# Performance work log

Hardware: AMD Instinct MI355X
Metric: run time of the kernel (lower is better)

Reference implementation:

```python
import jax, jax.numpy as jnp
import numpy as np

KH = KW = 3
STRIDE = 1
PAD = 1
DIL = 1


def im2col(x, kh, kw, stride, pad, dil):
    """F.unfold equivalent: x (N,C,H,W) -> (N,C,kh,kw,oh,ow)."""
    n, c, h, w = x.shape
    oh = (h + 2 * pad - dil * (kh - 1) - 1) // stride + 1
    ow = (w + 2 * pad - dil * (kw - 1) - 1) // stride + 1
    xp = jnp.pad(x, ((0, 0), (0, 0), (pad, pad), (pad, pad)))
    rows = []
    for i in range(kh):
        cols = []
        for j in range(kw):
            patch = jax.lax.slice(
                xp,
                (0, 0, i * dil, j * dil),
                (n, c, i * dil + (oh - 1) * stride + 1, j * dil + (ow - 1) * stride + 1),
                (1, 1, stride, stride),
            )  # (N,C,oh,ow)
            cols.append(patch)
        rows.append(jnp.stack(cols, axis=2))  # (N,C,kw,oh,ow)
    return jnp.stack(rows, axis=2)  # (N,C,kh,kw,oh,ow)


def setup_inputs() -> dict:
    key = jax.random.key(0)
    k1, k2, k3, k4 = jax.random.split(key, 4)
    N, Cin, Cout, H, W = 4, 64, 64, 128, 128
    x = jax.random.normal(k1, (N, Cin, H, W), dtype=jnp.float32)
    # adapting kernel: positive values (softmax-like output in EdgeKernel2d)
    kernel = jax.random.uniform(k2, (N, 1, KH, KW, H, W), dtype=jnp.float32, minval=0.01, maxval=1.0)
    fan_in = Cin * KH * KW
    weight = jax.random.normal(k3, (Cout, Cin, KH, KW), dtype=jnp.float32) * (1.0 / np.sqrt(fan_in))
    bias = jax.random.normal(k4, (Cout,), dtype=jnp.float32) * 0.01
    return {"x": x, "kernel": kernel, "weight": weight, "bias": bias}


def reference(x, kernel, weight, bias):
    # im_cols: (N,Cin,kh,kw,oh,ow)
    im_cols = im2col(x, KH, KW, STRIDE, PAD, DIL)
    in_mul_k = im_cols * kernel  # kernel broadcasts over Cin
    # dominate = sum_{k,l} in_mul_k / sum_{k,l} kernel  -> (N,Cin,oh,ow)
    dominate = in_mul_k.sum(axis=(2, 3)) / kernel.sum(axis=(2, 3))
    corrected = in_mul_k + dominate[:, :, None, None] * (1.0 - kernel)
    out = jnp.einsum('ncklhw,ockl->nohw', corrected, weight)
    out = out + bias[None, :, None, None]
    return out
```

## Files before the change

kernel.cpp:

```cpp
#include <hip/hip_runtime.h>
#include <cstddef>
#include <cstdint>

typedef __attribute__((ext_vector_type(8))) short bf16x8;
typedef __attribute__((ext_vector_type(4))) short short4v;
typedef __attribute__((ext_vector_type(4))) float f32x4;

#define NB 4
#define CIN 64
#define COUT 64
#define HH 128
#define WW 128
#define TAPS 9
#define PX 64
#define CCH 16
#define KCH 160
#define KTOT 640
#define STR 164

__device__ __forceinline__ unsigned short f2bf(float f) {
    union { float f; unsigned u; } v; v.f = f;
    unsigned u = v.u + 0x7FFFu + ((v.u >> 16) & 1u);
    return (unsigned short)(u >> 16);
}

__global__ void prep_weight(const float* __restrict__ w, unsigned short* __restrict__ wB) {
    int idx = blockIdx.x * blockDim.x + threadIdx.x;
    if (idx >= COUT * KTOT) return;
    int o = idx / KTOT;
    int kk = idx - o * KTOT;
    int chunk = kk / KCH;
    int kl = kk - chunk * KCH;
    unsigned short v = 0;
    if (kl < CCH * TAPS) {
        int tap = kl >> 4;
        int cl = kl & 15;
        int c = chunk * CCH + cl;
        v = f2bf(w[(o * CIN + c) * TAPS + tap]);
    }
    wB[idx] = v;
}

__launch_bounds__(256)
__global__ void pac_conv(const float* __restrict__ x, const float* __restrict__ Kp,
                         const unsigned short* __restrict__ wB,
                         const float* __restrict__ bias, float* __restrict__ out) {
    __shared__ __align__(16) unsigned short sCorT[PX][STR];
    __shared__ float sK[TAPS][PX];
    __shared__ float sInv[PX];

    const int blk = blockIdx.x;
    const int w0 = (blk & 1) * PX;
    const int h = (blk >> 1) & (HH - 1);
    const int n = blk >> 8;

    const int t = threadIdx.x;
    const int lane = t & 63;
    const int wv = t >> 6;
    const int spx = lane;

    for (int i = t; i < TAPS * PX; i += 256) {
        int tap = i >> 6, px = i & 63;
        sK[tap][px] = Kp[((n * TAPS + tap) * HH + h) * WW + w0 + px];
    }
    for (int i = t; i < PX * 16; i += 256) {
        sCorT[i >> 4][144 + (i & 15)] = 0;
    }
    __syncthreads();
    if (t < PX) {
        float s = 0.f;
        #pragma unroll
        for (int tap = 0; tap < TAPS; ++tap) s += sK[tap][t];
        sInv[t] = 1.0f / s;
    }
    __syncthreads();

    float kreg[TAPS];
    #pragma unroll
    for (int tap = 0; tap < TAPS; ++tap) kreg[tap] = sK[tap][spx];
    const float inv = sInv[spx];

    f32x4 acc[4];
    #pragma unroll
    for (int i = 0; i < 4; ++i) acc[i] = (f32x4){0.f, 0.f, 0.f, 0.f};

    const int o0 = wv * 16;
    const int l15 = lane & 15;
    const int kg = (lane >> 4) * 8;

    for (int chunk = 0; chunk < 4; ++chunk) {
        __syncthreads();
        const int cbase = chunk * CCH;
        #pragma unroll
        for (int it = 0; it < 4; ++it) {
            const int cl = wv + it * 4;
            const float* xb = x + (size_t)(n * CIN + cbase + cl) * (HH * WW);
            float xv[TAPS];
            float s1 = 0.f;
            #pragma unroll
            for (int k = 0; k < 3; ++k) {
                const int hh = h + k - 1;
                const bool hok = (unsigned)hh < (unsigned)HH;
                #pragma unroll
                for (int l = 0; l < 3; ++l) {
                    const int wc = w0 + spx + l - 1;
                    const bool ok = hok && ((unsigned)wc < (unsigned)WW);
                    float v = ok ? xb[hh * WW + wc] : 0.f;
                    xv[k * 3 + l] = v;
                    s1 = fmaf(v, kreg[k * 3 + l], s1);
                }
            }
            const float dom = s1 * inv;
            #pragma unroll
            for (int tap = 0; tap < TAPS; ++tap) {
                sCorT[spx][tap * 16 + cl] = f2bf(fmaf(kreg[tap], xv[tap] - dom, dom));
            }
        }
        __syncthreads();

        const unsigned short* wrow = wB + (size_t)(o0 + l15) * KTOT + chunk * KCH + kg;
        #pragma unroll
        for (int step = 0; step < 5; ++step) {
            const int k0 = step * 32;
            bf16x8 bfrag = *reinterpret_cast<const bf16x8*>(wrow + k0);
            #pragma unroll
            for (int pt = 0; pt < 4; ++pt) {
                const unsigned short* ap = &sCorT[pt * 16 + l15][k0 + kg];
                short4v alo = *reinterpret_cast<const short4v*>(ap);
                short4v ahi = *reinterpret_cast<const short4v*>(ap + 4);
                bf16x8 afrag;
                #pragma unroll
                for (int j = 0; j < 4; ++j) { afrag[j] = alo[j]; afrag[4 + j] = ahi[j]; }
                acc[pt] = __builtin_amdgcn_mfma_f32_16x16x32_bf16(afrag, bfrag, acc[pt], 0, 0, 0);
            }
        }
    }

    __syncthreads();
    float* sOut = reinterpret_cast<float*>(&sCorT[0][0]);
    #pragma unroll
    for (int pt = 0; pt < 4; ++pt) {
        #pragma unroll
        for (int r = 0; r < 4; ++r) {
            const int px = pt * 16 + (lane >> 4) * 4 + r;
            sOut[(o0 + l15) * 65 + px] = acc[pt][r];
        }
    }
    __syncthreads();
    #pragma unroll
    for (int j = 0; j < 16; ++j) {
        const int o = wv * 16 + j;
        out[(((size_t)n * COUT + o) * HH + h) * WW + w0 + spx] = sOut[o * 65 + spx] + bias[o];
    }
}

extern "C" void kernel_launch(void* const* d_in, const int* in_sizes, int n_in,
                              void* d_out, int out_size, void* d_ws, size_t ws_size,
                              hipStream_t stream) {
    const float* x    = (const float*)d_in[0];
    const float* Kp   = (const float*)d_in[1];
    const float* wgt  = (const float*)d_in[2];
    const float* bias = (const float*)d_in[3];
    float* out = (float*)d_out;
    unsigned short* wB = (unsigned short*)d_ws;

    prep_weight<<<(COUT * KTOT + 255) / 256, 256, 0, stream>>>(wgt, wB);

    pac_conv<<<NB * HH * (WW / PX), 256, 0, stream>>>(x, Kp, wB, bias, out);
}
```

Baseline: 33.78 us.

## Batch input loads per wave, pack bf16 pairs, and store MFMA results directly

Each wave now loads four channels at once with branch-free offset loads. Out-of-bounds rows read from a zeroed workspace row and the border columns are masked. The correction values are packed as bf16 pairs and written to shared memory as 8-byte stores, with one barrier per chunk. Kernel-weight loading and the normalisation sum are done per thread in registers, and the LDS transpose epilogue is dropped in favour of direct vectorized output stores with bias. This reduces barriers and LDS traffic and raises occupancy via launch bounds, at the cost of more registers per thread.

```diff
diff --git a/kernel.cpp b/kernel.cpp
--- a/kernel.cpp
+++ b/kernel.cpp
@@ -1,10 +1,10 @@
 #include <hip/hip_runtime.h>
+#include <hip/hip_bf16.h>
 #include <cstddef>
-#include <cstdint>
 
 typedef __attribute__((ext_vector_type(8))) short bf16x8;
-typedef __attribute__((ext_vector_type(4))) short short4v;
 typedef __attribute__((ext_vector_type(4))) float f32x4;
+typedef __attribute__((ext_vector_type(2))) unsigned int u32x2;
 
 #define NB 4
 #define CIN 64
@@ -13,10 +13,9 @@
 #define WW 128
 #define TAPS 9
 #define PX 64
-#define CCH 16
 #define KCH 160
 #define KTOT 640
-#define STR 164
+#define STRD 82
 
 __device__ __forceinline__ unsigned short f2bf(float f) {
     union { float f; unsigned u; } v; v.f = f;
@@ -24,133 +23,139 @@
     return (unsigned short)(u >> 16);
 }
 
-__global__ void prep_weight(const float* __restrict__ w, unsigned short* __restrict__ wB) {
+__global__ void prep_weight(const float* __restrict__ w, unsigned short* __restrict__ wB,
+                            float* __restrict__ zrow) {
     int idx = blockIdx.x * blockDim.x + threadIdx.x;
+    if (idx < 68) zrow[idx] = 0.f;
     if (idx >= COUT * KTOT) return;
     int o = idx / KTOT;
     int kk = idx - o * KTOT;
     int chunk = kk / KCH;
     int kl = kk - chunk * KCH;
     unsigned short v = 0;
-    if (kl < CCH * TAPS) {
+    if (kl < 16 * TAPS) {
         int tap = kl >> 4;
         int cl = kl & 15;
-        int c = chunk * CCH + cl;
-        v = f2bf(w[(o * CIN + c) * TAPS + tap]);
+        v = f2bf(w[(o * CIN + chunk * 16 + cl) * TAPS + tap]);
     }
     wB[idx] = v;
 }
 
-__launch_bounds__(256)
+__launch_bounds__(256, 4)
 __global__ void pac_conv(const float* __restrict__ x, const float* __restrict__ Kp,
                          const unsigned short* __restrict__ wB,
-                         const float* __restrict__ bias, float* __restrict__ out) {
-    __shared__ __align__(16) unsigned short sCorT[PX][STR];
-    __shared__ float sK[TAPS][PX];
-    __shared__ float sInv[PX];
+                         const float* __restrict__ bias,
+                         const float* __restrict__ zrow1,
+                         float* __restrict__ out) {
+    __shared__ unsigned int sCor[PX][STRD];
 
     const int blk = blockIdx.x;
     const int w0 = (blk & 1) * PX;
-    const int h = (blk >> 1) & (HH - 1);
-    const int n = blk >> 8;
-
-    const int t = threadIdx.x;
+    const int h  = (blk >> 1) & (HH - 1);
+    const int n  = blk >> 8;
+    const int t    = threadIdx.x;
     const int lane = t & 63;
-    const int wv = t >> 6;
-    const int spx = lane;
-
-    for (int i = t; i < TAPS * PX; i += 256) {
-        int tap = i >> 6, px = i & 63;
-        sK[tap][px] = Kp[((n * TAPS + tap) * HH + h) * WW + w0 + px];
-    }
-    for (int i = t; i < PX * 16; i += 256) {
-        sCorT[i >> 4][144 + (i & 15)] = 0;
-    }
-    __syncthreads();
-    if (t < PX) {
-        float s = 0.f;
-        #pragma unroll
-        for (int tap = 0; tap < TAPS; ++tap) s += sK[tap][t];
-        sInv[t] = 1.0f / s;
-    }
-    __syncthreads();
+    const int wv   = __builtin_amdgcn_readfirstlane(t >> 6);
 
     float kreg[TAPS];
+    float ks = 0.f;
+    const float* kp = Kp + ((size_t)n * TAPS * HH + h) * WW + w0 + lane;
     #pragma unroll
-    for (int tap = 0; tap < TAPS; ++tap) kreg[tap] = sK[tap][spx];
-    const float inv = sInv[spx];
+    for (int tap = 0; tap < TAPS; ++tap) {
+        kreg[tap] = kp[(size_t)tap * HH * WW];
+        ks += kreg[tap];
+    }
+    const float inv = 1.0f / ks;
+
+    for (int i = t; i < PX * 8; i += 256) sCor[i >> 3][72 + (i & 7)] = 0u;
+
+    const bool mL = (w0 == 0) && (lane == 0);
+    const bool mR = (w0 != 0) && (lane == 63);
+    const unsigned voffL = (mL ? 1u : (unsigned)lane) * 4u;
+    const unsigned voffC = ((unsigned)lane + 1u) * 4u;
+    const unsigned voffR = (mR ? 64u : (unsigned)lane + 2u) * 4u;
+
+    const int l15 = lane & 15;
+    const int kg  = (lane >> 4) * 8;
+    const float bval = bias[wv * 16 + l15];
 
     f32x4 acc[4];
     #pragma unroll
     for (int i = 0; i < 4; ++i) acc[i] = (f32x4){0.f, 0.f, 0.f, 0.f};
 
-    const int o0 = wv * 16;
-    const int l15 = lane & 15;
-    const int kg = (lane >> 4) * 8;
+    for (int chunk = 0; chunk < 4; ++chunk) {
+        const int c0 = chunk * 16 + wv * 4;
+        const float* xb = x + (size_t)(n * CIN + c0) * (HH * WW) + w0 - 1;
 
-    for (int chunk = 0; chunk < 4; ++chunk) {
-        __syncthreads();
-        const int cbase = chunk * CCH;
+        float xv[4][TAPS];
         #pragma unroll
-        for (int it = 0; it < 4; ++it) {
-            const int cl = wv + it * 4;
-            const float* xb = x + (size_t)(n * CIN + cbase + cl) * (HH * WW);
-            float xv[TAPS];
-            float s1 = 0.f;
+        for (int k = 0; k < 3; ++k) {
+            const int hh = h + k - 1;
+            const bool hok = (unsigned)hh < (unsigned)HH;
             #pragma unroll
-            for (int k = 0; k < 3; ++k) {
-                const int hh = h + k - 1;
-                const bool hok = (unsigned)hh < (unsigned)HH;
-                #pragma unroll
-                for (int l = 0; l < 3; ++l) {
-                    const int wc = w0 + spx + l - 1;
-                    const bool ok = hok && ((unsigned)wc < (unsigned)WW);
-                    float v = ok ? xb[hh * WW + wc] : 0.f;
-                    xv[k * 3 + l] = v;
-                    s1 = fmaf(v, kreg[k * 3 + l], s1);
-                }
-            }
-            const float dom = s1 * inv;
-            #pragma unroll
-            for (int tap = 0; tap < TAPS; ++tap) {
-                sCorT[spx][tap * 16 + cl] = f2bf(fmaf(kreg[tap], xv[tap] - dom, dom));
+            for (int j = 0; j < 4; ++j) {
+                const float* p = hok ? (xb + (size_t)j * (HH * WW) + hh * WW) : (zrow1 - 1);
+                float vL = *(const float*)((const char*)p + voffL);
+                float vC = *(const float*)((const char*)p + voffC);
+                float vR = *(const float*)((const char*)p + voffR);
+                xv[j][k * 3 + 0] = mL ? 0.f : vL;
+                xv[j][k * 3 + 1] = vC;
+                xv[j][k * 3 + 2] = mR ? 0.f : vR;
             }
         }
+
+        u32x2 cor[TAPS];
+        float dom[4];
+        #pragma unroll
+        for (int j = 0; j < 4; ++j) {
+            float s = 0.f;
+            #pragma unroll
+            for (int tap = 0; tap < TAPS; ++tap) s = fmaf(xv[j][tap], kreg[tap], s);
+            dom[j] = s * inv;
+        }
+        #pragma unroll
+        for (int tap = 0; tap < TAPS; ++tap) {
+            float c01[4];
+            #pragma unroll
+            for (int j = 0; j < 4; ++j)
+                c01[j] = fmaf(kreg[tap], xv[j][tap] - dom[j], dom[j]);
+            union { __hip_bfloat162 h2; unsigned int u; } a, b;
+            a.h2 = __float22bfloat162_rn(make_float2(c01[0], c01[1]));
+            b.h2 = __float22bfloat162_rn(make_float2(c01[2], c01[3]));
+            cor[tap] = (u32x2){a.u, b.u};
+        }
+
+        if (chunk) __syncthreads();
+        #pragma unroll
+        for (int tap = 0; tap < TAPS; ++tap)
+            *reinterpret_cast<u32x2*>(&sCor[lane][tap * 8 + wv * 2]) = cor[tap];
         __syncthreads();
 
-        const unsigned short* wrow = wB + (size_t)(o0 + l15) * KTOT + chunk * KCH + kg;
+        const unsigned short* wrow = wB + (size_t)(wv * 16 + l15) * KTOT + chunk * KCH + kg;
         #pragma unroll
         for (int step = 0; step < 5; ++step) {
-            const int k0 = step * 32;
-            bf16x8 bfrag = *reinterpret_cast<const bf16x8*>(wrow + k0);
+            bf16x8 bfrag = *reinterpret_cast<const bf16x8*>(wrow + step * 32);
             #pragma unroll
             for (int pt = 0; pt < 4; ++pt) {
-                const unsigned short* ap = &sCorT[pt * 16 + l15][k0 + kg];
-                short4v alo = *reinterpret_cast<const short4v*>(ap);
-                short4v ahi = *reinterpret_cast<const short4v*>(ap + 4);
-                bf16x8 afrag;
-                #pragma unroll
-                for (int j = 0; j < 4; ++j) { afrag[j] = alo[j]; afrag[4 + j] = ahi[j]; }
-                acc[pt] = __builtin_amdgcn_mfma_f32_16x16x32_bf16(afrag, bfrag, acc[pt], 0, 0, 0);
+                const unsigned int* ap = &sCor[pt * 16 + l15][(step * 32 + kg) >> 1];
+                u32x2 alo = *reinterpret_cast<const u32x2*>(ap);
+                u32x2 ahi = *reinterpret_cast<const u32x2*>(ap + 2);
+                union { u32x2 p[2]; bf16x8 f; } af;
+                af.p[0] = alo; af.p[1] = ahi;
+                acc[pt] = __builtin_amdgcn_mfma_f32_16x16x32_bf16(af.f, bfrag, acc[pt], 0, 0, 0);
             }
         }
     }
 
-    __syncthreads();
-    float* sOut = reinterpret_cast<float*>(&sCorT[0][0]);
+    const int o = wv * 16 + l15;
+    const int pxq = (lane >> 4) * 4;
+    float* op = out + (((size_t)n * COUT + o) * HH + h) * WW + w0 + pxq;
     #pragma unroll
     for (int pt = 0; pt < 4; ++pt) {
+        f32x4 v = acc[pt];
         #pragma unroll
-        for (int r = 0; r < 4; ++r) {
-            const int px = pt * 16 + (lane >> 4) * 4 + r;
-            sOut[(o0 + l15) * 65 + px] = acc[pt][r];
-        }
-    }
-    __syncthreads();
-    #pragma unroll
-    for (int j = 0; j < 16; ++j) {
-        const int o = wv * 16 + j;
-        out[(((size_t)n * COUT + o) * HH + h) * WW + w0 + spx] = sOut[o * 65 + spx] + bias[o];
+        for (int r = 0; r < 4; ++r) v[r] += bval;
+        *reinterpret_cast<f32x4*>(op + pt * 16) = v;
     }
 }
 
@@ -163,8 +168,9 @@
     const float* bias = (const float*)d_in[3];
     float* out = (float*)d_out;
     unsigned short* wB = (unsigned short*)d_ws;
+    float* zrow = (float*)((char*)d_ws + 81920);
 
-    prep_weight<<<(COUT * KTOT + 255) / 256, 256, 0, stream>>>(wgt, wB);
+    prep_weight<<<(COUT * KTOT + 255) / 256, 256, 0, stream>>>(wgt, wB, zrow);
 
-    pac_conv<<<NB * HH * (WW / PX), 256, 0, stream>>>(x, Kp, wB, bias, out);
+    pac_conv<<<NB * HH * (WW / PX), 256, 0, stream>>>(x, Kp, wB, bias, zrow + 1, out);
 }
```

Result: faster. 30.65 us (-9.3%).
